# Performance work log

Hardware: AMD Instinct MI355X
Metric: run time of the kernel (lower is better)

## Reference

```python
import jax, jax.numpy as jnp
import numpy as np

B, T, CF, D, H, HD, L, HID = 32, 384, 128, 512, 16, 32, 16, 512
EPS = 1e-6

def _make_pe():
    pos = np.arange(T, dtype=np.float32)[:, None]
    div = np.exp(np.arange(0, D, 2, dtype=np.float32) * (-np.log(10000.0) / D))
    pe = np.zeros((T, D), dtype=np.float32)
    pe[:, 0::2] = np.sin(pos * div)
    pe[:, 1::2] = np.cos(pos * div)
    return jnp.asarray(pe)

def setup_inputs() -> dict:
    key = jax.random.key(0)
    ks = jax.random.split(key, 12)
    n = lambda k, shp: jax.random.normal(k, shp, dtype=jnp.float32) * 0.02
    return {
        "index": jax.random.normal(ks[0], (B, T, CF), dtype=jnp.float32),
        "targets": jax.random.normal(ks[1], (B, T, CF), dtype=jnp.float32),
        "W_embed": n(ks[2], (CF, D)), "b_embed": jnp.zeros((D,), jnp.float32),
        "pe": _make_pe(), "learnable_pe": jnp.zeros((T, D), jnp.float32),
        "Wq": n(ks[3], (L, H, D, HD)), "Wk": n(ks[4], (L, H, D, HD)), "Wv": n(ks[5], (L, H, D, HD)),
        "Wproj": n(ks[6], (L, D, D)), "bproj": jnp.zeros((L, D), jnp.float32),
        "ln1_g": jnp.ones((L, D), jnp.float32), "ln1_b": jnp.zeros((L, D), jnp.float32),
        "ln2_g": jnp.ones((L, D), jnp.float32), "ln2_b": jnp.zeros((L, D), jnp.float32),
        "W1": n(ks[7], (L, D, HID)), "b1": jnp.zeros((L, HID), jnp.float32),
        "W2": n(ks[8], (L, HID, D)), "b2": jnp.zeros((L, D), jnp.float32),
        "W_final": n(ks[9], (D, CF)), "b_final": jnp.zeros((CF,), jnp.float32),
    }

def _ln(x, g, b):
    m = jnp.mean(x, axis=-1, keepdims=True)
    v = jnp.mean(jnp.square(x - m), axis=-1, keepdims=True)
    return (x - m) / jnp.sqrt(v + EPS) * g + b

def reference(index, targets, W_embed, b_embed, pe, learnable_pe,
              Wq, Wk, Wv, Wproj, bproj, ln1_g, ln1_b, ln2_g, ln2_b,
              W1, b1, W2, b2, W_final, b_final):
    mask = jnp.tril(jnp.ones((T, T), dtype=bool))
    # NOTE: original scales by 1/sqrt(C) where C = n_embed (input dim), not head_size
    scale = 1.0 / jnp.sqrt(jnp.float32(D))
    x = index @ W_embed + b_embed          # [B,T,D]
    x = x + pe + learnable_pe

    def blk(x, p):
        wq, wk, wv, wp, bp, g1, bl1, g2, bl2, w1, bb1, w2, bb2 = p
        h = _ln(x, g1, bl1)
        q = jnp.einsum('btc,hcd->bhtd', h, wq)
        k = jnp.einsum('btc,hcd->bhtd', h, wk)
        v = jnp.einsum('btc,hcd->bhtd', h, wv)
        s = jnp.einsum('bhtd,bhsd->bhts', q, k) * scale   # [B,H,T,T]
        s = jnp.where(mask, s, -jnp.inf)
        w = jax.nn.softmax(s, axis=-1)
        o = jnp.einsum('bhts,bhsd->bhtd', w, v)
        o = o.transpose(0, 2, 1, 3).reshape(x.shape[0], T, H * HD)
        x = x + o @ wp + bp                                # attn residual (dropout=eval)
        h2 = _ln(x, g2, bl2)
        x = x + jax.nn.relu(h2 @ w1 + bb1) @ w2 + bb2      # FFN residual
        return x, None

    x, _ = jax.lax.scan(blk, x, (Wq, Wk, Wv, Wproj, bproj, ln1_g, ln1_b,
                                 ln2_g, ln2_b, W1, b1, W2, b2))
    logits = x @ W_final + b_final         # [B,T,CF]
    loss = jnp.mean(jnp.square(logits - targets))
    return logits, loss
```

## Files before the change

kernel.cpp:

```cpp
#include <hip/hip_runtime.h>
#include <hip/hip_bf16.h>

#define B_   32
#define T_   384
#define CF_  128
#define D_   512
#define H_   16
#define HD_  32
#define L_   16
#define HID_ 512
#define M_   (B_*T_)

typedef __bf16 bf16x8 __attribute__((ext_vector_type(8)));
typedef float  f32x4  __attribute__((ext_vector_type(4)));

__device__ __forceinline__ float bf2f(unsigned short u){
    unsigned int x = ((unsigned int)u) << 16;
    return __builtin_bit_cast(float, x);
}
__device__ __forceinline__ unsigned short f2bf(float f){
    unsigned int u = __builtin_bit_cast(unsigned int, f);
    u += 0x7FFFu + ((u >> 16) & 1u);
    return (unsigned short)(u >> 16);
}
__device__ __forceinline__ unsigned int cvtpk(float lo, float hi){
    unsigned int r;
    asm("v_cvt_pk_bf16_f32 %0, %1, %2" : "=v"(r) : "v"(lo), "v"(hi));
    return r;
}

typedef const __attribute__((address_space(1))) unsigned int* gas_p;
typedef __attribute__((address_space(3))) unsigned int*       las_p;
__device__ __forceinline__ void gload16(const void* g, void* l){
    __builtin_amdgcn_global_load_lds((gas_p)g, (las_p)l, 16, 0, 0);
}

#define QSCALE 0.06376580687097174f

template<int EPI>
__global__ __launch_bounds__(256) void gemm_k(
    const unsigned short* __restrict__ A,
    const unsigned short* __restrict__ Bt,
    const float* __restrict__ aux0,
    const float* __restrict__ aux1,
    const float* __restrict__ aux2,
    float* __restrict__ fout,
    unsigned short* __restrict__ bout,
    int K)
{
    __shared__ unsigned short lA[2][128*32];
    __shared__ unsigned short lB[2][128*32];

    const int tid  = threadIdx.x;
    const int lane = tid & 63;
    const int w    = tid >> 6;
    const int wm   = w >> 1, wn = w & 1;
    const int li   = lane & 15, ls = lane >> 4;
    const int m0   = blockIdx.x * 128;
    const int n0   = blockIdx.y * 128;
    const int nkt  = K >> 5;

    const int e0 = tid, e1 = tid + 256;
    const int r0 = e0 >> 2, s0 = (e0 & 3) ^ ((r0 >> 1) & 3);
    const int r1 = e1 >> 2, s1 = (e1 & 3) ^ ((r1 >> 1) & 3);
    const unsigned short* gA0 = A  + (size_t)(m0 + r0)*K + s0*8;
    const unsigned short* gA1 = A  + (size_t)(m0 + r1)*K + s1*8;
    const unsigned short* gB0 = Bt + (size_t)(n0 + r0)*K + s0*8;
    const unsigned short* gB1 = Bt + (size_t)(n0 + r1)*K + s1*8;

#define STAGE(c, kt) do{ \
    const int ko_ = (kt)*32; \
    gload16(gA0 + ko_, &lA[c][w*512]); \
    gload16(gA1 + ko_, &lA[c][2048 + w*512]); \
    gload16(gB0 + ko_, &lB[c][w*512]); \
    gload16(gB1 + ko_, &lB[c][2048 + w*512]); \
}while(0)

    f32x4 acc[4][4];
    #pragma unroll
    for (int i=0;i<4;i++)
        #pragma unroll
        for (int j=0;j<4;j++) acc[i][j] = (f32x4){0.f,0.f,0.f,0.f};

    STAGE(0, 0);
    asm volatile("s_waitcnt vmcnt(0)" ::: "memory");
    __syncthreads();

    int cur = 0;
    for (int kt = 0; kt < nkt; ++kt){
        if (kt + 1 < nkt) STAGE(cur^1, kt+1);
        bf16x8 af[4], bf[4];
        #pragma unroll
        for (int f=0; f<4; ++f){
            const int rA = wm*64 + f*16 + li;
            af[f] = *(const bf16x8*)&lA[cur][rA*32 + ((ls ^ ((rA>>1)&3))*8)];
            const int rB = wn*64 + f*16 + li;
            bf[f] = *(const bf16x8*)&lB[cur][rB*32 + ((ls ^ ((rB>>1)&3))*8)];
        }
        #pragma unroll
        for (int i=0;i<4;i++)
            #pragma unroll
            for (int j=0;j<4;j++)
                acc[i][j] = __builtin_amdgcn_mfma_f32_16x16x32_bf16(af[i], bf[j], acc[i][j], 0, 0, 0);
        __syncthreads();
        cur ^= 1;
    }
#undef STAGE

    if constexpr (EPI == 1){
        #pragma unroll
        for (int i=0;i<4;i++){
            #pragma unroll
            for (int j=0;j<4;j++){
                const int row0 = m0 + wm*64 + i*16 + ls*4;
                const int col  = n0 + wn*64 + j*16 + li;
                const int mat = col >> 9, nl = col & 511;
                const int hh = nl >> 5, dd = nl & 31;
                const int bb = row0 / T_, tt0 = row0 - bb*T_;
                if (mat == 2){
                    alignas(8) unsigned short p4[4];
                    #pragma unroll
                    for (int t=0;t<4;t++) p4[t] = f2bf(acc[i][j][t]);
                    *(uint2*)(bout + 2*(size_t)(M_*D_)
                              + ((size_t)(bb*H_ + hh)*HD_ + dd)*T_ + tt0) = *(const uint2*)p4;
                } else {
                    #pragma unroll
                    for (int t=0;t<4;t++){
                        float v = acc[i][j][t];
                        if (mat == 0) v *= QSCALE;
                        bout[(size_t)mat*(M_*D_)
                             + (((size_t)(bb*H_ + hh)*T_ + tt0 + t)*HD_) + dd] = f2bf(v);
                    }
                }
            }
        }
    } else {
        #pragma unroll
        for (int i=0;i<4;i++){
            #pragma unroll
            for (int j=0;j<4;j++){
                #pragma unroll
                for (int t=0;t<4;t++){
                    const int row = m0 + wm*64 + i*16 + ls*4 + t;
                    const int col = n0 + wn*64 + j*16 + li;
                    const float v = acc[i][j][t];
                    if constexpr (EPI == 0){
                        const int tt = row % T_;
                        fout[row*D_ + col] = v + aux0[col] + aux1[tt*D_ + col] + aux2[tt*D_ + col];
                    } else if constexpr (EPI == 2){
                        fout[row*D_ + col] += v + aux0[col];
                    } else if constexpr (EPI == 3){
                        const float r = v + aux0[col];
                        bout[row*HID_ + col] = f2bf(r > 0.f ? r : 0.f);
                    } else {
                        fout[row*CF_ + col] = v + aux0[col];
                    }
                }
            }
        }
    }
}

__global__ __launch_bounds__(256) void ln_k(const float* __restrict__ x,
                                            const float* __restrict__ g,
                                            const float* __restrict__ b,
                                            unsigned short* __restrict__ out)
{
    const int w = threadIdx.x >> 6, lane = threadIdx.x & 63;
    const int row = blockIdx.x*4 + w;
    const float* xr = x + (size_t)row*D_;
    const float4 a = *(const float4*)(xr + lane*8);
    const float4 c = *(const float4*)(xr + lane*8 + 4);
    float s  = a.x+a.y+a.z+a.w + c.x+c.y+c.z+c.w;
    float q2 = a.x*a.x+a.y*a.y+a.z*a.z+a.w*a.w + c.x*c.x+c.y*c.y+c.z*c.z+c.w*c.w;
    #pragma unroll
    for (int off=32; off; off>>=1){
        s  += __shfl_xor(s,  off);
        q2 += __shfl_xor(q2, off);
    }
    const float mean = s * (1.f/512.f);
    const float var  = q2 * (1.f/512.f) - mean*mean;
    const float rstd = rsqrtf(var + 1e-6f);
    const float4 gA = *(const float4*)(g + lane*8);
    const float4 gB = *(const float4*)(g + lane*8 + 4);
    const float4 bA = *(const float4*)(b + lane*8);
    const float4 bB = *(const float4*)(b + lane*8 + 4);
    alignas(16) unsigned short o8[8];
    o8[0] = f2bf((a.x-mean)*rstd*gA.x + bA.x);
    o8[1] = f2bf((a.y-mean)*rstd*gA.y + bA.y);
    o8[2] = f2bf((a.z-mean)*rstd*gA.z + bA.z);
    o8[3] = f2bf((a.w-mean)*rstd*gA.w + bA.w);
    o8[4] = f2bf((c.x-mean)*rstd*gB.x + bB.x);
    o8[5] = f2bf((c.y-mean)*rstd*gB.y + bB.y);
    o8[6] = f2bf((c.z-mean)*rstd*gB.z + bB.z);
    o8[7] = f2bf((c.w-mean)*rstd*gB.w + bB.w);
    *(uint4*)(out + (size_t)row*D_ + lane*8) = *(const uint4*)o8;
}

__global__ __launch_bounds__(256) void attn_k(const unsigned short* __restrict__ q,
                                              const unsigned short* __restrict__ k,
                                              const unsigned short* __restrict__ vt,
                                              unsigned short* __restrict__ o)
{
    __shared__ unsigned int Pb[4][2*16*18];

    const int orig = blockIdx.x;
    const int wg   = (orig & 7)*192 + (orig >> 3);
    const int bh   = wg / 3;
    const int t0   = (wg - bh*3) * 128;

    const int tid  = threadIdx.x;
    const int lane = tid & 63, w = tid >> 6;
    const int li   = lane & 15, ls = lane >> 4;
    const unsigned short* qb = q  + (size_t)bh*(T_*HD_);
    const unsigned short* kb = k  + (size_t)bh*(T_*HD_);
    const unsigned short* vb = vt + (size_t)bh*(HD_*T_);

    const int trow0 = t0 + w*32;
    const bf16x8 qaA = *(const bf16x8*)(qb + (trow0 + li)*HD_ + ls*8);
    const bf16x8 qaB = *(const bf16x8*)(qb + (trow0 + 16 + li)*HD_ + ls*8);
    const int nfull = trow0 >> 5;

    float lsA = 0.f, lsB = 0.f;
    f32x4 oA0={0.f,0.f,0.f,0.f}, oA1={0.f,0.f,0.f,0.f};
    f32x4 oB0={0.f,0.f,0.f,0.f}, oB1={0.f,0.f,0.f,0.f};
    unsigned int* pwA = Pb[w];
    unsigned int* pwB = Pb[w] + 288;

    bf16x8 kf0 = *(const bf16x8*)(kb + li*HD_ + ls*8);
    bf16x8 kf1 = *(const bf16x8*)(kb + (16 + li)*HD_ + ls*8);
    bf16x8 vf0 = *(const bf16x8*)(vb + li*T_ + ls*8);
    bf16x8 vf1 = *(const bf16x8*)(vb + (16 + li)*T_ + ls*8);

    for (int c = 0; c < nfull; ++c){
        f32x4 sA0={0.f,0.f,0.f,0.f}, sA1={0.f,0.f,0.f,0.f};
        f32x4 sB0={0.f,0.f,0.f,0.f}, sB1={0.f,0.f,0.f,0.f};
        sA0 = __builtin_amdgcn_mfma_f32_16x16x32_bf16(kf0, qaA, sA0, 0, 0, 0);
        sA1 = __builtin_amdgcn_mfma_f32_16x16x32_bf16(kf1, qaA, sA1, 0, 0, 0);
        sB0 = __builtin_amdgcn_mfma_f32_16x16x32_bf16(kf0, qaB, sB0, 0, 0, 0);
        sB1 = __builtin_amdgcn_mfma_f32_16x16x32_bf16(kf1, qaB, sB1, 0, 0, 0);
        kf0 = *(const bf16x8*)(kb + ((c+1)*32 + li)*HD_ + ls*8);
        kf1 = *(const bf16x8*)(kb + ((c+1)*32 + 16 + li)*HD_ + ls*8);

        float pA0[4], pA1[4], pB0[4], pB1[4];
        #pragma unroll
        for (int j=0;j<4;j++){
            pA0[j] = exp2f(sA0[j]); pA1[j] = exp2f(sA1[j]);
            pB0[j] = exp2f(sB0[j]); pB1[j] = exp2f(sB1[j]);
        }
        lsA += pA0[0]+pA0[1]+pA0[2]+pA0[3]+pA1[0]+pA1[1]+pA1[2]+pA1[3];
        lsB += pB0[0]+pB0[1]+pB0[2]+pB0[3]+pB1[0]+pB1[1]+pB1[2]+pB1[3];

        const uint2 wA0 = { cvtpk(pA0[0], pA0[1]), cvtpk(pA0[2], pA0[3]) };
        const uint2 wA1 = { cvtpk(pA1[0], pA1[1]), cvtpk(pA1[2], pA1[3]) };
        const uint2 wB0 = { cvtpk(pB0[0], pB0[1]), cvtpk(pB0[2], pB0[3]) };
        const uint2 wB1 = { cvtpk(pB1[0], pB1[1]), cvtpk(pB1[2], pB1[3]) };
        *(uint2*)&pwA[li*18 + ls*2]     = wA0;
        *(uint2*)&pwA[li*18 + 8 + ls*2] = wA1;
        *(uint2*)&pwB[li*18 + ls*2]     = wB0;
        *(uint2*)&pwB[li*18 + 8 + ls*2] = wB1;
        asm volatile("s_waitcnt lgkmcnt(0)" ::: "memory");
        const bf16x8 paA = *(const bf16x8*)&pwA[li*18 + ls*4];
        const bf16x8 paB = *(const bf16x8*)&pwB[li*18 + ls*4];

        oA0 = __builtin_amdgcn_mfma_f32_16x16x32_bf16(paA, vf0, oA0, 0, 0, 0);
        oA1 = __builtin_amdgcn_mfma_f32_16x16x32_bf16(paA, vf1, oA1, 0, 0, 0);
        oB0 = __builtin_amdgcn_mfma_f32_16x16x32_bf16(paB, vf0, oB0, 0, 0, 0);
        oB1 = __builtin_amdgcn_mfma_f32_16x16x32_bf16(paB, vf1, oB1, 0, 0, 0);
        vf0 = *(const bf16x8*)(vb + li*T_ + (c+1)*32 + ls*8);
        vf1 = *(const bf16x8*)(vb + (16 + li)*T_ + (c+1)*32 + ls*8);
    }

    {
        f32x4 sA0={0.f,0.f,0.f,0.f}, sB0={0.f,0.f,0.f,0.f}, sB1={0.f,0.f,0.f,0.f};
        sA0 = __builtin_amdgcn_mfma_f32_16x16x32_bf16(kf0, qaA, sA0, 0, 0, 0);
        sB0 = __builtin_amdgcn_mfma_f32_16x16x32_bf16(kf0, qaB, sB0, 0, 0, 0);
        sB1 = __builtin_amdgcn_mfma_f32_16x16x32_bf16(kf1, qaB, sB1, 0, 0, 0);

        const int qA = li, qB = 16 + li;
        float pA0[4], pB0[4], pB1[4];
        #pragma unroll
        for (int j=0;j<4;j++){
            const int k0 = ls*4 + j;
            pA0[j] = (k0 <= qA)      ? exp2f(sA0[j]) : 0.f;
            pB0[j] = exp2f(sB0[j]);
            pB1[j] = (k0 + 16 <= qB) ? exp2f(sB1[j]) : 0.f;
        }
        lsA += pA0[0]+pA0[1]+pA0[2]+pA0[3];
        lsB += pB0[0]+pB0[1]+pB0[2]+pB0[3]+pB1[0]+pB1[1]+pB1[2]+pB1[3];

        const uint2 wA0 = { cvtpk(pA0[0], pA0[1]), cvtpk(pA0[2], pA0[3]) };
        const uint2 wB0 = { cvtpk(pB0[0], pB0[1]), cvtpk(pB0[2], pB0[3]) };
        const uint2 wB1 = { cvtpk(pB1[0], pB1[1]), cvtpk(pB1[2], pB1[3]) };
        const uint2 zz  = { 0u, 0u };
        *(uint2*)&pwA[li*18 + ls*2]     = wA0;
        *(uint2*)&pwA[li*18 + 8 + ls*2] = zz;
        *(uint2*)&pwB[li*18 + ls*2]     = wB0;
        *(uint2*)&pwB[li*18 + 8 + ls*2] = wB1;
        asm volatile("s_waitcnt lgkmcnt(0)" ::: "memory");
        const bf16x8 paA = *(const bf16x8*)&pwA[li*18 + ls*4];
        const bf16x8 paB = *(const bf16x8*)&pwB[li*18 + ls*4];

        oA0 = __builtin_amdgcn_mfma_f32_16x16x32_bf16(paA, vf0, oA0, 0, 0, 0);
        oA1 = __builtin_amdgcn_mfma_f32_16x16x32_bf16(paA, vf1, oA1, 0, 0, 0);
        oB0 = __builtin_amdgcn_mfma_f32_16x16x32_bf16(paB, vf0, oB0, 0, 0, 0);
        oB1 = __builtin_amdgcn_mfma_f32_16x16x32_bf16(paB, vf1, oB1, 0, 0, 0);
    }

    lsA += __shfl_xor(lsA, 16);  lsA += __shfl_xor(lsA, 32);
    lsB += __shfl_xor(lsB, 16);  lsB += __shfl_xor(lsB, 32);

    const int bb = bh >> 4, hh = bh & 15;
    #pragma unroll
    for (int j=0;j<4;j++){
        const float rsA = __shfl(lsA, ls*4 + j);
        const float rsB = __shfl(lsB, ls*4 + j);
        const float iA = 1.f / rsA, iB = 1.f / rsB;
        const int tgA = trow0 + ls*4 + j;
        const int tgB = tgA + 16;
        o[(size_t)(bb*T_ + tgA)*D_ + hh*HD_ + li]      = f2bf(oA0[j]*iA);
        o[(size_t)(bb*T_ + tgA)*D_ + hh*HD_ + 16 + li] = f2bf(oA1[j]*iA);
        o[(size_t)(bb*T_ + tgB)*D_ + hh*HD_ + li]      = f2bf(oB0[j]*iB);
        o[(size_t)(bb*T_ + tgB)*D_ + hh*HD_ + 16 + li] = f2bf(oB1[j]*iB);
    }
}

__global__ __launch_bounds__(256) void packT_k(const float* __restrict__ src,
                                               unsigned short* __restrict__ dst,
                                               int R, int C)
{
    __shared__ unsigned short tile[64][72];
    const int z  = blockIdx.z;
    const float* s = src + (size_t)z*R*C;
    unsigned short* d = dst + (size_t)z*R*C;
    const int c0 = blockIdx.x*64, r0 = blockIdx.y*64;

    for (int it = threadIdx.x; it < 1024; it += 256){
        const int rr  = it >> 4;
        const int cc4 = (it & 15) << 2;
        const float4 v = *(const float4*)(s + (size_t)(r0+rr)*C + c0 + cc4);
        tile[cc4  ][rr] = f2bf(v.x);
        tile[cc4+1][rr] = f2bf(v.y);
        tile[cc4+2][rr] = f2bf(v.z);
        tile[cc4+3][rr] = f2bf(v.w);
    }
    __syncthreads();
    for (int it = threadIdx.x; it < 512; it += 256){
        const int cc = it >> 3;
        const int ch = (it & 7) << 3;
        *(uint4*)(d + (size_t)(c0+cc)*R + r0 + ch) = *(const uint4*)&tile[cc][ch];
    }
}

__global__ __launch_bounds__(256) void pack_qkv_k(const float* __restrict__ Wq,
                                                  const float* __restrict__ Wk,
                                                  const float* __restrict__ Wv,
                                                  unsigned short* __restrict__ dst)
{
    __shared__ unsigned short tile[32][136];
    const int kc  = blockIdx.x;
    const int mat = blockIdx.y >> 4;
    const int h   = blockIdx.y & 15;
    const int l   = blockIdx.z;
    const float* src = ((mat==0) ? Wq : (mat==1) ? Wk : Wv)
                     + ((size_t)(l*H_ + h)*D_ + kc*128)*HD_;

    for (int it = threadIdx.x; it < 1024; it += 256){
        const int rr  = it >> 3;
        const int dd4 = (it & 7) << 2;
        const float4 v = *(const float4*)(src + (size_t)rr*HD_ + dd4);
        tile[dd4  ][rr] = f2bf(v.x);
        tile[dd4+1][rr] = f2bf(v.y);
        tile[dd4+2][rr] = f2bf(v.z);
        tile[dd4+3][rr] = f2bf(v.w);
    }
    __syncthreads();
    unsigned short* dp = dst + (size_t)l*786432 + (size_t)mat*262144 + kc*128;
    for (int it = threadIdx.x; it < 512; it += 256){
        const int dd = it >> 4;
        const int ch = (it & 15) << 3;
        *(uint4*)(dp + (size_t)(h*32 + dd)*512 + ch) = *(const uint4*)&tile[dd][ch];
    }
}

__global__ void cast4_k(const float* __restrict__ src, unsigned short* __restrict__ dst, int total4)
{
    const int i = blockIdx.x*256 + threadIdx.x;
    if (i >= total4) return;
    const float4 vv = ((const float4*)src)[i];
    alignas(8) unsigned short t[4] = { f2bf(vv.x), f2bf(vv.y), f2bf(vv.z), f2bf(vv.w) };
    *(uint2*)(dst + (size_t)i*4) = *(const uint2*)t;
}

__global__ __launch_bounds__(256) void loss1_k(const float* __restrict__ logits,
                                               const float* __restrict__ tgt,
                                               float* __restrict__ part)
{
    float s = 0.f;
    for (int i = blockIdx.x*256 + threadIdx.x; i < M_*CF_; i += 256*1024){
        const float d = logits[i] - tgt[i];
        s += d*d;
    }
    #pragma unroll
    for (int off=32; off; off>>=1) s += __shfl_xor(s, off);
    __shared__ float ws4[4];
    if ((threadIdx.x & 63) == 0) ws4[threadIdx.x >> 6] = s;
    __syncthreads();
    if (threadIdx.x == 0) part[blockIdx.x] = ws4[0]+ws4[1]+ws4[2]+ws4[3];
}

__global__ __launch_bounds__(256) void loss2_k(const float* __restrict__ part,
                                               float* __restrict__ out)
{
    float s = 0.f;
    for (int i = threadIdx.x; i < 1024; i += 256) s += part[i];
    #pragma unroll
    for (int off=32; off; off>>=1) s += __shfl_xor(s, off);
    __shared__ float ws4[4];
    if ((threadIdx.x & 63) == 0) ws4[threadIdx.x >> 6] = s;
    __syncthreads();
    if (threadIdx.x == 0) out[0] = (ws4[0]+ws4[1]+ws4[2]+ws4[3]) * (1.f/(float)(M_*CF_));
}

static constexpr size_t X_OFF     = 0;
static constexpr size_t H_OFF     = 25165824;
static constexpr size_t O_OFF     = 37748736;
static constexpr size_t QKV_OFF   = 50331648;
static constexpr size_t WQKV_OFF  = 88080384;
static constexpr size_t WPROJ_OFF = 113246208;
static constexpr size_t W1_OFF    = 121634816;
static constexpr size_t W2_OFF    = 130023424;
static constexpr size_t WEMB_OFF  = 138412032;
static constexpr size_t WFIN_OFF  = 138543104;
static constexpr size_t PART_OFF  = 138674176;

extern "C" void kernel_launch(void* const* d_in, const int* in_sizes, int n_in,
                              void* d_out, int out_size, void* d_ws, size_t ws_size,
                              hipStream_t stream)
{
    const float* index   = (const float*)d_in[0];
    const float* targets = (const float*)d_in[1];
    const float* W_embed = (const float*)d_in[2];
    const float* b_embed = (const float*)d_in[3];
    const float* pe      = (const float*)d_in[4];
    const float* lpe     = (const float*)d_in[5];
    const float* Wq      = (const float*)d_in[6];
    const float* Wk      = (const float*)d_in[7];
    const float* Wv      = (const float*)d_in[8];
    const float* Wproj   = (const float*)d_in[9];
    const float* bproj   = (const float*)d_in[10];
    const float* ln1g    = (const float*)d_in[11];
    const float* ln1b    = (const float*)d_in[12];
    const float* ln2g    = (const float*)d_in[13];
    const float* ln2b    = (const float*)d_in[14];
    const float* W1      = (const float*)d_in[15];
    const float* b1      = (const float*)d_in[16];
    const float* W2      = (const float*)d_in[17];
    const float* b2      = (const float*)d_in[18];
    const float* Wfin    = (const float*)d_in[19];
    const float* bfin    = (const float*)d_in[20];

    char* ws = (char*)d_ws;
    float*          x     = (float*)(ws + X_OFF);
    unsigned short* hbuf  = (unsigned short*)(ws + H_OFF);
    unsigned short* obuf  = (unsigned short*)(ws + O_OFF);
    unsigned short* qkv   = (unsigned short*)(ws + QKV_OFF);
    unsigned short* wqkvp = (unsigned short*)(ws + WQKV_OFF);
    unsigned short* wprojp= (unsigned short*)(ws + WPROJ_OFF);
    unsigned short* w1p   = (unsigned short*)(ws + W1_OFF);
    unsigned short* w2p   = (unsigned short*)(ws + W2_OFF);
    unsigned short* wembp = (unsigned short*)(ws + WEMB_OFF);
    unsigned short* wfinp = (unsigned short*)(ws + WFIN_OFF);
    float*          part  = (float*)(ws + PART_OFF);
    float*          logits= (float*)d_out;

    pack_qkv_k<<<dim3(4,48,16), 256, 0, stream>>>(Wq, Wk, Wv, wqkvp);
    packT_k<<<dim3(8,8,16), 256, 0, stream>>>(Wproj, wprojp, 512, 512);
    packT_k<<<dim3(8,8,16), 256, 0, stream>>>(W1,    w1p,    512, 512);
    packT_k<<<dim3(8,8,16), 256, 0, stream>>>(W2,    w2p,    512, 512);
    packT_k<<<dim3(8,2,1),  256, 0, stream>>>(W_embed, wembp, 128, 512);
    packT_k<<<dim3(2,8,1),  256, 0, stream>>>(Wfin,    wfinp, 512, 128);

    cast4_k<<<1536, 256, 0, stream>>>(index, obuf, 393216);
    gemm_k<0><<<dim3(96,4), 256, 0, stream>>>(obuf, wembp, b_embed, pe, lpe, x, nullptr, 128);

    for (int l = 0; l < L_; ++l){
        ln_k<<<3072, 256, 0, stream>>>(x, ln1g + l*512, ln1b + l*512, hbuf);
        gemm_k<1><<<dim3(96,12), 256, 0, stream>>>(hbuf, wqkvp + (size_t)l*786432,
                                                   nullptr, nullptr, nullptr, nullptr, qkv, 512);
        attn_k<<<1536, 256, 0, stream>>>(qkv, qkv + 6291456, qkv + 2*6291456, obuf);
        gemm_k<2><<<dim3(96,4), 256, 0, stream>>>(obuf, wprojp + (size_t)l*262144,
                                                  bproj + l*512, nullptr, nullptr, x, nullptr, 512);
        ln_k<<<3072, 256, 0, stream>>>(x, ln2g + l*512, ln2b + l*512, hbuf);
        gemm_k<3><<<dim3(96,4), 256, 0, stream>>>(hbuf, w1p + (size_t)l*262144,
                                                  b1 + l*512, nullptr, nullptr, nullptr, obuf, 512);
        gemm_k<2><<<dim3(96,4), 256, 0, stream>>>(obuf, w2p + (size_t)l*262144,
                                                  b2 + l*512, nullptr, nullptr, x, nullptr, 512);
    }

    cast4_k<<<6144, 256, 0, stream>>>(x, hbuf, 1572864);
    gemm_k<4><<<dim3(96,1), 256, 0, stream>>>(hbuf, wfinp, bfin, nullptr, nullptr, logits, nullptr, 512);
    loss1_k<<<1024, 256, 0, stream>>>(logits, targets, part);
    loss2_k<<<1, 256, 0, stream>>>(part, logits + 1572864);
}
```

Before: 2.076 ms.

## Use 128x192 tile GEMM for QKV and double-buffer K/V fragments in attention

Adds a dedicated QKV projection kernel with 128x192 output tiles (4x6 MFMA fragments per wave), launching 768 blocks instead of 1152. Each A tile is now reused across more columns, which cuts A reloads and block count. The attention kernel also prefetches K/V fragments two chunks ahead into register double buffers to hide global load latency. In exchange the new GEMM uses more accumulator registers and more LDS, which may lower occupancy.

Result: slower. 3.935 ms (+89.6%).

```diff
diff --git a/kernel.cpp b/kernel.cpp
--- a/kernel.cpp
+++ b/kernel.cpp
@@ -107,54 +107,128 @@
     }
 #undef STAGE
 
-    if constexpr (EPI == 1){
-        #pragma unroll
-        for (int i=0;i<4;i++){
+    #pragma unroll
+    for (int i=0;i<4;i++){
+        #pragma unroll
+        for (int j=0;j<4;j++){
             #pragma unroll
-            for (int j=0;j<4;j++){
-                const int row0 = m0 + wm*64 + i*16 + ls*4;
-                const int col  = n0 + wn*64 + j*16 + li;
-                const int mat = col >> 9, nl = col & 511;
-                const int hh = nl >> 5, dd = nl & 31;
-                const int bb = row0 / T_, tt0 = row0 - bb*T_;
-                if (mat == 2){
-                    alignas(8) unsigned short p4[4];
-                    #pragma unroll
-                    for (int t=0;t<4;t++) p4[t] = f2bf(acc[i][j][t]);
-                    *(uint2*)(bout + 2*(size_t)(M_*D_)
-                              + ((size_t)(bb*H_ + hh)*HD_ + dd)*T_ + tt0) = *(const uint2*)p4;
+            for (int t=0;t<4;t++){
+                const int row = m0 + wm*64 + i*16 + ls*4 + t;
+                const int col = n0 + wn*64 + j*16 + li;
+                const float v = acc[i][j][t];
+                if constexpr (EPI == 0){
+                    const int tt = row % T_;
+                    fout[row*D_ + col] = v + aux0[col] + aux1[tt*D_ + col] + aux2[tt*D_ + col];
+                } else if constexpr (EPI == 2){
+                    fout[row*D_ + col] += v + aux0[col];
+                } else if constexpr (EPI == 3){
+                    const float r = v + aux0[col];
+                    bout[row*HID_ + col] = f2bf(r > 0.f ? r : 0.f);
                 } else {
-                    #pragma unroll
-                    for (int t=0;t<4;t++){
-                        float v = acc[i][j][t];
-                        if (mat == 0) v *= QSCALE;
-                        bout[(size_t)mat*(M_*D_)
-                             + (((size_t)(bb*H_ + hh)*T_ + tt0 + t)*HD_) + dd] = f2bf(v);
-                    }
+                    fout[row*CF_ + col] = v + aux0[col];
                 }
             }
         }
-    } else {
-        #pragma unroll
-        for (int i=0;i<4;i++){
+    }
+}
+
+__global__ __launch_bounds__(256) void gemm192_k(
+    const unsigned short* __restrict__ A,
+    const unsigned short* __restrict__ Bt,
+    unsigned short* __restrict__ bout,
+    int K)
+{
+    __shared__ unsigned short lA[2][128*32];
+    __shared__ unsigned short lB[2][192*32];
+
+    const int tid  = threadIdx.x;
+    const int lane = tid & 63;
+    const int w    = tid >> 6;
+    const int wm   = w >> 1, wn = w & 1;
+    const int li   = lane & 15, ls = lane >> 4;
+    const int m0   = blockIdx.x * 128;
+    const int n0   = blockIdx.y * 192;
+    const int nkt  = K >> 5;
+
+    const int ea0 = tid, ea1 = tid + 256;
+    const int ra0 = ea0 >> 2, sa0 = (ea0 & 3) ^ ((ra0 >> 1) & 3);
+    const int ra1 = ea1 >> 2, sa1 = (ea1 & 3) ^ ((ra1 >> 1) & 3);
+    const unsigned short* gA0 = A + (size_t)(m0 + ra0)*K + sa0*8;
+    const unsigned short* gA1 = A + (size_t)(m0 + ra1)*K + sa1*8;
+
+    const int eb0 = tid, eb1 = tid + 256, eb2 = tid + 512;
+    const int rb0 = eb0 >> 2, sb0 = (eb0 & 3) ^ ((rb0 >> 1) & 3);
+    const int rb1 = eb1 >> 2, sb1 = (eb1 & 3) ^ ((rb1 >> 1) & 3);
+    const int rb2 = eb2 >> 2, sb2 = (eb2 & 3) ^ ((rb2 >> 1) & 3);
+    const unsigned short* gB0 = Bt + (size_t)(n0 + rb0)*K + sb0*8;
+    const unsigned short* gB1 = Bt + (size_t)(n0 + rb1)*K + sb1*8;
+    const unsigned short* gB2 = Bt + (size_t)(n0 + rb2)*K + sb2*8;
+
+#define STAGE192(c, kt) do{ \
+    const int ko_ = (kt)*32; \
+    gload16(gA0 + ko_, &lA[c][w*512]); \
+    gload16(gA1 + ko_, &lA[c][2048 + w*512]); \
+    gload16(gB0 + ko_, &lB[c][w*512]); \
+    gload16(gB1 + ko_, &lB[c][2048 + w*512]); \
+    gload16(gB2 + ko_, &lB[c][4096 + w*512]); \
+}while(0)
+
+    f32x4 acc[4][6];
+    #pragma unroll
+    for (int i=0;i<4;i++)
+        #pragma unroll
+        for (int j=0;j<6;j++) acc[i][j] = (f32x4){0.f,0.f,0.f,0.f};
+
+    STAGE192(0, 0);
+    asm volatile("s_waitcnt vmcnt(0)" ::: "memory");
+    __syncthreads();
+
+    int cur = 0;
+    for (int kt = 0; kt < nkt; ++kt){
+        if (kt + 1 < nkt) STAGE192(cur^1, kt+1);
+        bf16x8 af[4], bf[6];
+        #pragma unroll
+        for (int f=0; f<4; ++f){
+            const int rA = wm*64 + f*16 + li;
+            af[f] = *(const bf16x8*)&lA[cur][rA*32 + ((ls ^ ((rA>>1)&3))*8)];
+        }
+        #pragma unroll
+        for (int f=0; f<6; ++f){
+            const int rB = wn*96 + f*16 + li;
+            bf[f] = *(const bf16x8*)&lB[cur][rB*32 + ((ls ^ ((rB>>1)&3))*8)];
+        }
+        #pragma unroll
+        for (int i=0;i<4;i++)
             #pragma unroll
-            for (int j=0;j<4;j++){
+            for (int j=0;j<6;j++)
+                acc[i][j] = __builtin_amdgcn_mfma_f32_16x16x32_bf16(af[i], bf[j], acc[i][j], 0, 0, 0);
+        __syncthreads();
+        cur ^= 1;
+    }
+#undef STAGE192
+
+    #pragma unroll
+    for (int i=0;i<4;i++){
+        #pragma unroll
+        for (int j=0;j<6;j++){
+            const int row0 = m0 + wm*64 + i*16 + ls*4;
+            const int col  = n0 + wn*96 + j*16 + li;
+            const int mat = col >> 9, nl = col & 511;
+            const int hh = nl >> 5, dd = nl & 31;
+            const int bb = row0 / T_, tt0 = row0 - bb*T_;
+            if (mat == 2){
+                alignas(8) unsigned short p4[4];
+                #pragma unroll
+                for (int t=0;t<4;t++) p4[t] = f2bf(acc[i][j][t]);
+                *(uint2*)(bout + 2*(size_t)(M_*D_)
+                          + ((size_t)(bb*H_ + hh)*HD_ + dd)*T_ + tt0) = *(const uint2*)p4;
+            } else {
                 #pragma unroll
                 for (int t=0;t<4;t++){
-                    const int row = m0 + wm*64 + i*16 + ls*4 + t;
-                    const int col = n0 + wn*64 + j*16 + li;
-                    const float v = acc[i][j][t];
-                    if constexpr (EPI == 0){
-                        const int tt = row % T_;
-                        fout[row*D_ + col] = v + aux0[col] + aux1[tt*D_ + col] + aux2[tt*D_ + col];
-                    } else if constexpr (EPI == 2){
-                        fout[row*D_ + col] += v + aux0[col];
-                    } else if constexpr (EPI == 3){
-                        const float r = v + aux0[col];
-                        bout[row*HID_ + col] = f2bf(r > 0.f ? r : 0.f);
-                    } else {
-                        fout[row*CF_ + col] = v + aux0[col];
-                    }
+                    float v = acc[i][j][t];
+                    if (mat == 0) v *= QSCALE;
+                    bout[(size_t)mat*(M_*D_)
+                         + (((size_t)(bb*H_ + hh)*T_ + tt0 + t)*HD_) + dd] = f2bf(v);
                 }
             }
         }
@@ -227,20 +301,31 @@
     unsigned int* pwA = Pb[w];
     unsigned int* pwB = Pb[w] + 288;
 
-    bf16x8 kf0 = *(const bf16x8*)(kb + li*HD_ + ls*8);
-    bf16x8 kf1 = *(const bf16x8*)(kb + (16 + li)*HD_ + ls*8);
-    bf16x8 vf0 = *(const bf16x8*)(vb + li*T_ + ls*8);
-    bf16x8 vf1 = *(const bf16x8*)(vb + (16 + li)*T_ + ls*8);
+    bf16x8 kf0[2], kf1[2], vf0[2], vf1[2];
+    {
+        const int i1 = (1 <= nfull) ? 1 : nfull;
+        kf0[0] = *(const bf16x8*)(kb + li*HD_ + ls*8);
+        kf1[0] = *(const bf16x8*)(kb + (16 + li)*HD_ + ls*8);
+        vf0[0] = *(const bf16x8*)(vb + li*T_ + ls*8);
+        vf1[0] = *(const bf16x8*)(vb + (16 + li)*T_ + ls*8);
+        kf0[1] = *(const bf16x8*)(kb + (i1*32 + li)*HD_ + ls*8);
+        kf1[1] = *(const bf16x8*)(kb + (i1*32 + 16 + li)*HD_ + ls*8);
+        vf0[1] = *(const bf16x8*)(vb + li*T_ + i1*32 + ls*8);
+        vf1[1] = *(const bf16x8*)(vb + (16 + li)*T_ + i1*32 + ls*8);
+    }
 
     for (int c = 0; c < nfull; ++c){
+        const int sl = c & 1;
         f32x4 sA0={0.f,0.f,0.f,0.f}, sA1={0.f,0.f,0.f,0.f};
         f32x4 sB0={0.f,0.f,0.f,0.f}, sB1={0.f,0.f,0.f,0.f};
-        sA0 = __builtin_amdgcn_mfma_f32_16x16x32_bf16(kf0, qaA, sA0, 0, 0, 0);
-        sA1 = __builtin_amdgcn_mfma_f32_16x16x32_bf16(kf1, qaA, sA1, 0, 0, 0);
-        sB0 = __builtin_amdgcn_mfma_f32_16x16x32_bf16(kf0, qaB, sB0, 0, 0, 0);
-        sB1 = __builtin_amdgcn_mfma_f32_16x16x32_bf16(kf1, qaB, sB1, 0, 0, 0);
-        kf0 = *(const bf16x8*)(kb + ((c+1)*32 + li)*HD_ + ls*8);
-        kf1 = *(const bf16x8*)(kb + ((c+1)*32 + 16 + li)*HD_ + ls*8);
+        sA0 = __builtin_amdgcn_mfma_f32_16x16x32_bf16(kf0[sl], qaA, sA0, 0, 0, 0);
+        sA1 = __builtin_amdgcn_mfma_f32_16x16x32_bf16(kf1[sl], qaA, sA1, 0, 0, 0);
+        sB0 = __builtin_amdgcn_mfma_f32_16x16x32_bf16(kf0[sl], qaB, sB0, 0, 0, 0);
+        sB1 = __builtin_amdgcn_mfma_f32_16x16x32_bf16(kf1[sl], qaB, sB1, 0, 0, 0);
+        if (c + 2 <= nfull){
+            kf0[sl] = *(const bf16x8*)(kb + ((c+2)*32 + li)*HD_ + ls*8);
+            kf1[sl] = *(const bf16x8*)(kb + ((c+2)*32 + 16 + li)*HD_ + ls*8);
+        }
 
         float pA0[4], pA1[4], pB0[4], pB1[4];
         #pragma unroll
@@ -263,19 +348,22 @@
         const bf16x8 paA = *(const bf16x8*)&pwA[li*18 + ls*4];
         const bf16x8 paB = *(const bf16x8*)&pwB[li*18 + ls*4];
 
-        oA0 = __builtin_amdgcn_mfma_f32_16x16x32_bf16(paA, vf0, oA0, 0, 0, 0);
-        oA1 = __builtin_amdgcn_mfma_f32_16x16x32_bf16(paA, vf1, oA1, 0, 0, 0);
-        oB0 = __builtin_amdgcn_mfma_f32_16x16x32_bf16(paB, vf0, oB0, 0, 0, 0);
-        oB1 = __builtin_amdgcn_mfma_f32_16x16x32_bf16(paB, vf1, oB1, 0, 0, 0);
-        vf0 = *(const bf16x8*)(vb + li*T_ + (c+1)*32 + ls*8);
-        vf1 = *(const bf16x8*)(vb + (16 + li)*T_ + (c+1)*32 + ls*8);
+        oA0 = __builtin_amdgcn_mfma_f32_16x16x32_bf16(paA, vf0[sl], oA0, 0, 0, 0);
+        oA1 = __builtin_amdgcn_mfma_f32_16x16x32_bf16(paA, vf1[sl], oA1, 0, 0, 0);
+        oB0 = __builtin_amdgcn_mfma_f32_16x16x32_bf16(paB, vf0[sl], oB0, 0, 0, 0);
+        oB1 = __builtin_amdgcn_mfma_f32_16x16x32_bf16(paB, vf1[sl], oB1, 0, 0, 0);
+        if (c + 2 <= nfull){
+            vf0[sl] = *(const bf16x8*)(vb + li*T_ + (c+2)*32 + ls*8);
+            vf1[sl] = *(const bf16x8*)(vb + (16 + li)*T_ + (c+2)*32 + ls*8);
+        }
     }
 
     {
+        const int sl = nfull & 1;
         f32x4 sA0={0.f,0.f,0.f,0.f}, sB0={0.f,0.f,0.f,0.f}, sB1={0.f,0.f,0.f,0.f};
-        sA0 = __builtin_amdgcn_mfma_f32_16x16x32_bf16(kf0, qaA, sA0, 0, 0, 0);
-        sB0 = __builtin_amdgcn_mfma_f32_16x16x32_bf16(kf0, qaB, sB0, 0, 0, 0);
-        sB1 = __builtin_amdgcn_mfma_f32_16x16x32_bf16(kf1, qaB, sB1, 0, 0, 0);
+        sA0 = __builtin_amdgcn_mfma_f32_16x16x32_bf16(kf0[sl], qaA, sA0, 0, 0, 0);
+        sB0 = __builtin_amdgcn_mfma_f32_16x16x32_bf16(kf0[sl], qaB, sB0, 0, 0, 0);
+        sB1 = __builtin_amdgcn_mfma_f32_16x16x32_bf16(kf1[sl], qaB, sB1, 0, 0, 0);
 
         const int qA = li, qB = 16 + li;
         float pA0[4], pB0[4], pB1[4];
@@ -301,10 +389,10 @@
         const bf16x8 paA = *(const bf16x8*)&pwA[li*18 + ls*4];
         const bf16x8 paB = *(const bf16x8*)&pwB[li*18 + ls*4];
 
-        oA0 = __builtin_amdgcn_mfma_f32_16x16x32_bf16(paA, vf0, oA0, 0, 0, 0);
-        oA1 = __builtin_amdgcn_mfma_f32_16x16x32_bf16(paA, vf1, oA1, 0, 0, 0);
-        oB0 = __builtin_amdgcn_mfma_f32_16x16x32_bf16(paB, vf0, oB0, 0, 0, 0);
-        oB1 = __builtin_amdgcn_mfma_f32_16x16x32_bf16(paB, vf1, oB1, 0, 0, 0);
+        oA0 = __builtin_amdgcn_mfma_f32_16x16x32_bf16(paA, vf0[sl], oA0, 0, 0, 0);
+        oA1 = __builtin_amdgcn_mfma_f32_16x16x32_bf16(paA, vf1[sl], oA1, 0, 0, 0);
+        oB0 = __builtin_amdgcn_mfma_f32_16x16x32_bf16(paB, vf0[sl], oB0, 0, 0, 0);
+        oB1 = __builtin_amdgcn_mfma_f32_16x16x32_bf16(paB, vf1[sl], oB1, 0, 0, 0);
     }
 
     lsA += __shfl_xor(lsA, 16);  lsA += __shfl_xor(lsA, 32);
@@ -486,8 +574,7 @@
 
     for (int l = 0; l < L_; ++l){
         ln_k<<<3072, 256, 0, stream>>>(x, ln1g + l*512, ln1b + l*512, hbuf);
-        gemm_k<1><<<dim3(96,12), 256, 0, stream>>>(hbuf, wqkvp + (size_t)l*786432,
-                                                   nullptr, nullptr, nullptr, nullptr, qkv, 512);
+        gemm192_k<<<dim3(96,8), 256, 0, stream>>>(hbuf, wqkvp + (size_t)l*786432, qkv, 512);
         attn_k<<<1536, 256, 0, stream>>>(qkv, qkv + 6291456, qkv + 2*6291456, obuf);
         gemm_k<2><<<dim3(96,4), 256, 0, stream>>>(obuf, wprojp + (size_t)l*262144,
                                                   bproj + l*512, nullptr, nullptr, x, nullptr, 512);
```
